# Kernel optimization log

Measured on AMD Instinct MI355X. Metric: run time of the kernel, lower is better.

Reference implementation:

```python
import jax, jax.numpy as jnp
import numpy as np

F_CNT, V_CNT = 1024, 512
H, W = 192, 192
FX, FY = 200.0, 200.0
CX, CY = W / 2.0, H / 2.0
EPS = 1e-8


def quat_to_rot(q):
    # WXYZ quaternion -> rotation matrix, with normalization.
    q = q / (jnp.linalg.norm(q, axis=-1, keepdims=True) + EPS)
    w, x, y, z = q[..., 0], q[..., 1], q[..., 2], q[..., 3]
    return jnp.stack([
        jnp.stack([1 - 2 * (y * y + z * z), 2 * (x * y - w * z), 2 * (x * z + w * y)], -1),
        jnp.stack([2 * (x * y + w * z), 1 - 2 * (x * x + z * z), 2 * (y * z - w * x)], -1),
        jnp.stack([2 * (x * z - w * y), 2 * (y * z + w * x), 1 - 2 * (x * x + y * y)], -1),
    ], -2)


def rot_to_quat(R):
    # Branchless rotation matrix -> WXYZ quaternion.
    m00, m11, m22 = R[..., 0, 0], R[..., 1, 1], R[..., 2, 2]
    qw = 0.5 * jnp.sqrt(jnp.maximum(EPS, 1 + m00 + m11 + m22))
    qx = 0.5 * jnp.sqrt(jnp.maximum(EPS, 1 + m00 - m11 - m22))
    qy = 0.5 * jnp.sqrt(jnp.maximum(EPS, 1 - m00 + m11 - m22))
    qz = 0.5 * jnp.sqrt(jnp.maximum(EPS, 1 - m00 - m11 + m22))
    qx = jnp.copysign(qx, R[..., 2, 1] - R[..., 1, 2])
    qy = jnp.copysign(qy, R[..., 0, 2] - R[..., 2, 0])
    qz = jnp.copysign(qz, R[..., 1, 0] - R[..., 0, 1])
    return jnp.stack([qw, qx, qy, qz], -1)


def get_face_coord(a, b, c):
    # Per-face orthonormal frame (columns = x,y,z axes) and centroid.
    t = (a + b + c) / 3.0
    e1, e2 = b - a, c - a
    x = e1 / (jnp.linalg.norm(e1, axis=-1, keepdims=True) + EPS)
    n = jnp.cross(e1, e2)
    z = n / (jnp.linalg.norm(n, axis=-1, keepdims=True) + EPS)
    y = jnp.cross(z, x)
    return jnp.stack([x, y, z], -1), t


def render_gaussians(means, rot_qs, scales, colors, opac):
    # Differentiable 3DGS-style render: project, build 2D conics, depth-sorted
    # alpha compositing over all gaussians per pixel, white background.
    Rn = quat_to_rot(rot_qs)                      # [F,3,3]
    M = Rn * scales[:, None, :]                   # R @ diag(s)
    cov3 = M @ jnp.swapaxes(M, -1, -2)            # [F,3,3]
    X, Y, Z = means[:, 0], means[:, 1], means[:, 2]
    valid = (Z > 0.2).astype(means.dtype)
    Zc = jnp.maximum(Z, 0.2)
    mx = FX * X / Zc + CX
    my = FY * Y / Zc + CY
    zero = jnp.zeros_like(Zc)
    J = jnp.stack([
        jnp.stack([FX / Zc, zero, -FX * X / (Zc * Zc)], -1),
        jnp.stack([zero, FY / Zc, -FY * Y / (Zc * Zc)], -1),
    ], -2)                                        # [F,2,3]
    cov2 = J @ cov3 @ jnp.swapaxes(J, -1, -2)     # [F,2,2]
    a = cov2[:, 0, 0] + 0.3                       # low-pass dilation (3DGS)
    b = cov2[:, 0, 1]
    c = cov2[:, 1, 1] + 0.3
    det = jnp.maximum(a * c - b * b, EPS)
    conA, conB, conC = c / det, -b / det, a / det
    ys, xs = jnp.meshgrid(jnp.arange(H, dtype=means.dtype),
                          jnp.arange(W, dtype=means.dtype), indexing='ij')
    px, py = xs.reshape(-1), ys.reshape(-1)       # [HW]
    dx = px[None, :] - mx[:, None]                # [F,HW]
    dy = py[None, :] - my[:, None]
    power = -0.5 * (conA[:, None] * dx * dx + conC[:, None] * dy * dy) - conB[:, None] * dx * dy
    alpha = jnp.clip(opac[:, None] * jnp.exp(jnp.minimum(power, 0.0)), 0.0, 0.99) * valid[:, None]
    order = jnp.argsort(Zc)                       # front-to-back
    alpha = alpha[order]
    cols = colors[order]
    T = jnp.cumprod(1.0 - alpha, axis=0)
    T_excl = jnp.concatenate([jnp.ones_like(T[:1]), T[:-1]], axis=0)
    w = alpha * T_excl                            # [F,HW]
    img = jnp.einsum('fp,fc->cp', w, cols) + (1.0 - jnp.sum(w, 0))[None, :]
    return img.reshape(colors.shape[1], H, W)


def setup_inputs() -> dict:
    ks = jax.random.split(jax.random.key(0), 8)
    vp = jax.random.normal(ks[0], (V_CNT, 3), jnp.float32) * 0.5
    vp = vp.at[:, 2].add(5.0)  # put the mesh in front of the camera
    return {
        'img': jax.random.uniform(ks[1], (3, H, W), jnp.float32),
        'mask': jax.random.uniform(ks[2], (H, W), jnp.float32),
        'vertex_positions': vp,
        'faces': jax.random.randint(ks[3], (F_CNT, 3), 0, V_CNT, jnp.int32),
        'gp_rot_qs': jax.random.normal(ks[4], (F_CNT, 4), jnp.float32),
        'gp_log_scales': jax.random.normal(ks[5], (F_CNT, 3), jnp.float32) * 0.1 - 3.0,
        'gp_colors': jax.random.uniform(ks[6], (F_CNT, 3), jnp.float32),
        'gp_log_opacities': jnp.zeros((F_CNT, 1), jnp.float32),
    }


def reference(img, mask, vertex_positions, faces, gp_rot_qs, gp_log_scales,
              gp_colors, gp_log_opacities):
    vps_a = vertex_positions[faces[:, 0]]
    vps_b = vertex_positions[faces[:, 1]]
    vps_c = vertex_positions[faces[:, 2]]
    face_rs, face_ts = get_face_coord(vps_a, vps_b, vps_c)      # [F,3,3],[F,3]
    gp_scales = jnp.exp(gp_log_scales)
    gp_rot_mats = quat_to_rot(gp_rot_qs)
    # rows = scaled columns of the rotation (exactly as the torch code stacks)
    gp_rs = jnp.stack([gp_rot_mats[:, :, 0] * gp_scales[:, 0:1],
                       gp_rot_mats[:, :, 1] * gp_scales[:, 1:2],
                       gp_rot_mats[:, :, 2] * gp_scales[:, 2:3]], -2)
    global_gp_rs = face_rs @ gp_rs                               # merge_rt, gp_t = 0
    global_gp_ts = face_ts
    global_scales = jnp.linalg.norm(global_gp_rs, axis=-2)      # column norms [F,3]
    global_rot = global_gp_rs / (global_scales[:, None, :] + EPS)
    global_qs = rot_to_quat(global_rot)
    opac = jnp.exp(gp_log_opacities)[:, 0]
    rendered = render_gaussians(global_gp_ts, global_qs, global_scales, gp_colors, opac)
    mask_ = mask[None]
    masked_img = (1.0 - mask_) + img * mask_                     # white bg composite
    rgb_loss = jnp.mean((rendered - masked_img) ** 2)
    return rendered, rgb_loss
```

## Files before the change

kernel.cpp:

```cpp
#include <hip/hip_runtime.h>
#include <hip/hip_fp16.h>
#include <math.h>

#define F_CNT 1024
#define H_IMG 192
#define W_IMG 192
#define HW (H_IMG * W_IMG)
#define EPSF 1e-8f
#define N_SEG 8
#define SEG_LEN 128
#define HALF_PX 72
#define PIX_PER_BLK 144
#define LOG2E 1.4426950408889634f

#define RCP(x) __builtin_amdgcn_rcpf(x)


__device__ __forceinline__ void bstep(unsigned long long &kv, int j, int k, int tid)
{
    const unsigned long long pk = __shfl_xor(kv, j, 64);
    const bool keep_min = (((tid & k) == 0) == ((tid & j) == 0));
    kv = ((pk < kv) == keep_min) ? pk : kv;
}

__global__ __launch_bounds__(1024)
void prep_sort_kernel(const float* __restrict__ vp,
                      const int*   __restrict__ faces,
                      const float* __restrict__ rot_qs,
                      const float* __restrict__ log_scales,
                      const float* __restrict__ colors,
                      const float* __restrict__ log_opac,
                      float* __restrict__ params,
                      float* __restrict__ out)
{
    __shared__ float sp[8][F_CNT];
    __shared__ unsigned long long skv[F_CNT];

    const int f = threadIdx.x;
    if (f == 0) out[3 * HW] = 0.0f;

    const int ia = faces[3 * f + 0], ib = faces[3 * f + 1], ic = faces[3 * f + 2];
    const float Ax = vp[3 * ia + 0], Ay = vp[3 * ia + 1], Az = vp[3 * ia + 2];
    const float Bx = vp[3 * ib + 0], By = vp[3 * ib + 1], Bz = vp[3 * ib + 2];
    const float Cx = vp[3 * ic + 0], Cy = vp[3 * ic + 1], Cz = vp[3 * ic + 2];

    const float tx = (Ax + Bx + Cx) / 3.0f;
    const float ty = (Ay + By + Cy) / 3.0f;
    const float tz = (Az + Bz + Cz) / 3.0f;

    const float e1x = Bx - Ax, e1y = By - Ay, e1z = Bz - Az;
    const float e2x = Cx - Ax, e2y = Cy - Ay, e2z = Cz - Az;

    const float rn1 = RCP(sqrtf(e1x * e1x + e1y * e1y + e1z * e1z) + EPSF);
    const float ux = e1x * rn1, uy = e1y * rn1, uz = e1z * rn1;
    const float cnx = e1y * e2z - e1z * e2y;
    const float cny = e1z * e2x - e1x * e2z;
    const float cnz = e1x * e2y - e1y * e2x;
    const float rn2 = RCP(sqrtf(cnx * cnx + cny * cny + cnz * cnz) + EPSF);
    const float wxv = cnx * rn2, wyv = cny * rn2, wzv = cnz * rn2;
    const float vx = wyv * uz - wzv * uy;
    const float vy = wzv * ux - wxv * uz;
    const float vz = wxv * uy - wyv * ux;

    const float q0 = rot_qs[4 * f + 0], q1 = rot_qs[4 * f + 1];
    const float q2 = rot_qs[4 * f + 2], q3 = rot_qs[4 * f + 3];
    const float rqn = RCP(sqrtf(q0 * q0 + q1 * q1 + q2 * q2 + q3 * q3) + EPSF);
    const float qw = q0 * rqn, qx = q1 * rqn, qy = q2 * rqn, qz = q3 * rqn;
    const float R00 = 1.0f - 2.0f * (qy * qy + qz * qz);
    const float R01 = 2.0f * (qx * qy - qw * qz);
    const float R02 = 2.0f * (qx * qz + qw * qy);
    const float R10 = 2.0f * (qx * qy + qw * qz);
    const float R11 = 1.0f - 2.0f * (qx * qx + qz * qz);
    const float R12 = 2.0f * (qy * qz - qw * qx);
    const float R20 = 2.0f * (qx * qz - qw * qy);
    const float R21 = 2.0f * (qy * qz + qw * qx);
    const float R22 = 1.0f - 2.0f * (qx * qx + qy * qy);

    const float s0 = expf(log_scales[3 * f + 0]);
    const float s1 = expf(log_scales[3 * f + 1]);
    const float s2 = expf(log_scales[3 * f + 2]);

    float G00, G10, G20, G01, G11, G21, G02, G12, G22;
    {
        float c0 = s0 * R00, c1 = s1 * R01, c2 = s2 * R02;
        G00 = ux * c0 + vx * c1 + wxv * c2;
        G10 = uy * c0 + vy * c1 + wyv * c2;
        G20 = uz * c0 + vz * c1 + wzv * c2;
    }
    {
        float c0 = s0 * R10, c1 = s1 * R11, c2 = s2 * R12;
        G01 = ux * c0 + vx * c1 + wxv * c2;
        G11 = uy * c0 + vy * c1 + wyv * c2;
        G21 = uz * c0 + vz * c1 + wzv * c2;
    }
    {
        float c0 = s0 * R20, c1 = s1 * R21, c2 = s2 * R22;
        G02 = ux * c0 + vx * c1 + wxv * c2;
        G12 = uy * c0 + vy * c1 + wyv * c2;
        G22 = uz * c0 + vz * c1 + wzv * c2;
    }

    const float gs0 = sqrtf(G00 * G00 + G10 * G10 + G20 * G20);
    const float gs1 = sqrtf(G01 * G01 + G11 * G11 + G21 * G21);
    const float gs2 = sqrtf(G02 * G02 + G12 * G12 + G22 * G22);
    const float rd0 = RCP(gs0 + EPSF), rd1 = RCP(gs1 + EPSF), rd2 = RCP(gs2 + EPSF);
    const float r00 = G00 * rd0, r10 = G10 * rd0, r20 = G20 * rd0;
    const float r01 = G01 * rd1, r11 = G11 * rd1, r21 = G21 * rd1;
    const float r02 = G02 * rd2, r12 = G12 * rd2, r22 = G22 * rd2;

    const float Qw = 0.5f * sqrtf(fmaxf(EPSF, 1.0f + r00 + r11 + r22));
    const float Qx = copysignf(0.5f * sqrtf(fmaxf(EPSF, 1.0f + r00 - r11 - r22)), r21 - r12);
    const float Qy = copysignf(0.5f * sqrtf(fmaxf(EPSF, 1.0f - r00 + r11 - r22)), r02 - r20);
    const float Qz = copysignf(0.5f * sqrtf(fmaxf(EPSF, 1.0f - r00 - r11 + r22)), r10 - r01);

    const float rqn2 = RCP(sqrtf(Qw * Qw + Qx * Qx + Qy * Qy + Qz * Qz) + EPSF);
    const float pw = Qw * rqn2, px = Qx * rqn2, py = Qy * rqn2, pz = Qz * rqn2;
    const float N00 = 1.0f - 2.0f * (py * py + pz * pz);
    const float N01 = 2.0f * (px * py - pw * pz);
    const float N02 = 2.0f * (px * pz + pw * py);
    const float N10 = 2.0f * (px * py + pw * pz);
    const float N11 = 1.0f - 2.0f * (px * px + pz * pz);
    const float N12 = 2.0f * (py * pz - pw * px);
    const float N20 = 2.0f * (px * pz - pw * py);
    const float N21 = 2.0f * (py * pz + pw * px);
    const float N22 = 1.0f - 2.0f * (px * px + py * py);

    const float M00 = N00 * gs0, M01 = N01 * gs1, M02 = N02 * gs2;
    const float M10 = N10 * gs0, M11 = N11 * gs1, M12 = N12 * gs2;
    const float M20 = N20 * gs0, M21 = N21 * gs1, M22 = N22 * gs2;
    const float C00 = M00 * M00 + M01 * M01 + M02 * M02;
    const float C01 = M00 * M10 + M01 * M11 + M02 * M12;
    const float C02 = M00 * M20 + M01 * M21 + M02 * M22;
    const float C11 = M10 * M10 + M11 * M11 + M12 * M12;
    const float C12 = M10 * M20 + M11 * M21 + M12 * M22;
    const float C22 = M20 * M20 + M21 * M21 + M22 * M22;

    const float valid = (tz > 0.2f) ? 1.0f : 0.0f;
    const float Zc = fmaxf(tz, 0.2f);
    const float rZc = RCP(Zc);
    const float mx = 200.0f * tx * rZc + 96.0f;
    const float my = 200.0f * ty * rZc + 96.0f;
    const float j00 = 200.0f * rZc;
    const float j02 = -200.0f * tx * (rZc * rZc);
    const float j11 = 200.0f * rZc;
    const float j12 = -200.0f * ty * (rZc * rZc);
    const float v00 = j00 * j00 * C00 + 2.0f * j00 * j02 * C02 + j02 * j02 * C22 + 0.3f;
    const float v01 = j00 * j11 * C01 + j00 * j12 * C02 + j02 * j11 * C12 + j02 * j12 * C22;
    const float v11 = j11 * j11 * C11 + 2.0f * j11 * j12 * C12 + j12 * j12 * C22 + 0.3f;
    const float rdet = RCP(fmaxf(v00 * v11 - v01 * v01, EPSF));
    const float conA = v11 * rdet, conB = -v01 * rdet, conC = v00 * rdet;
    const float opv = expf(log_opac[f]) * valid;

    const float LA = 0.5f * LOG2E * conA;
    const float LB = LOG2E * conB;
    const float LC = 0.5f * LOG2E * conC;
    const float t4 = fmaf(-LB, LB, 4.0f * LA * LC);
    const float reach2 = 140.0f * LA * RCP(fmaxf(t4, 1e-30f));

    union { __half2 h; float f; } c01u, cbo;
    c01u.h = __floats2half2_rn(colors[3 * f + 0], colors[3 * f + 1]);
    cbo.h  = __floats2half2_rn(colors[3 * f + 2], opv);

    sp[0][f] = mx;
    sp[1][f] = my;
    sp[2][f] = reach2;
    sp[3][f] = LA;
    sp[4][f] = LB;
    sp[5][f] = LC;
    sp[6][f] = c01u.f;
    sp[7][f] = cbo.f;

    unsigned long long kv =
        ((unsigned long long)__float_as_uint(Zc) << 32) | (unsigned int)f;

    #pragma unroll
    for (int k = 2; k <= 64; k <<= 1)
        #pragma unroll
        for (int j = k >> 1; j > 0; j >>= 1)
            bstep(kv, j, k, f);

    skv[f] = kv;
    __syncthreads();

    for (int k = 128; k <= F_CNT; k <<= 1) {
        for (int j = k >> 1; j >= 64; j >>= 1) {
            const int x = f ^ j;
            if (x > f) {
                const unsigned long long a  = skv[f];
                const unsigned long long bb = skv[x];
                const bool up = ((f & k) == 0);
                if (up ? (a > bb) : (a < bb)) { skv[f] = bb; skv[x] = a; }
            }
            __syncthreads();
        }
        kv = skv[f];
        #pragma unroll
        for (int j = 32; j > 0; j >>= 1)
            bstep(kv, j, k, f);
        skv[f] = kv;
        __syncthreads();
    }

    const int src = (int)(skv[f] & 0xffffffffULL);
    float4* __restrict__ d4 = (float4*)params + 2 * f;
    d4[0] = make_float4(sp[0][src], sp[1][src], sp[2][src], sp[3][src]);
    d4[1] = make_float4(sp[4][src], sp[5][src], sp[6][src], sp[7][src]);
}

__global__ __launch_bounds__(512)
void render_kernel(const float* __restrict__ params,
                   const float* __restrict__ img,
                   const float* __restrict__ mask,
                   float* __restrict__ out)
{
    __shared__ float4 lds4[F_CNT * 2];
    __shared__ float  lossb[PIX_PER_BLK];

    const int tid  = threadIdx.x;
    const int lane = tid & 63;
    const int wv   = tid >> 6;

    const float4* __restrict__ rec4 = (const float4*)params;
    #pragma unroll
    for (int k = 0; k < 4; ++k)
        lds4[k * 512 + tid] = rec4[k * 512 + tid];
    __syncthreads();

    const int b   = blockIdx.x;
    const int pb1 = b * HALF_PX;
    const int pb2 = HW / 2 + b * HALF_PX;

    const float r1a = (float)(pb1 / W_IMG);
    const float r1b = (float)((pb1 + HALF_PX - 1) / W_IMG);
    const float r2a = (float)(pb2 / W_IMG);
    const float r2b = (float)((pb2 + HALF_PX - 1) / W_IMG);

    const int p0 = pb1 + lane,      p1 = pb1 + 64 + lane;
    const int p2 = pb2 + lane,      p3 = pb2 + 64 + lane;
    const float fx0 = (float)(p0 % W_IMG), fy0 = (float)(p0 / W_IMG);
    const float fx1 = (float)(p1 % W_IMG), fy1 = (float)(p1 / W_IMG);
    const float fx2 = (float)(p2 % W_IMG), fy2 = (float)(p2 / W_IMG);
    const float fx3 = (float)(p3 % W_IMG), fy3 = (float)(p3 / W_IMG);

    float T0 = 1.0f, R0 = 0.0f, G0 = 0.0f, B0 = 0.0f;
    float T1 = 1.0f, R1 = 0.0f, G1 = 0.0f, B1 = 0.0f;
    float T2 = 1.0f, R2 = 0.0f, G2 = 0.0f, B2 = 0.0f;
    float T3 = 1.0f, R3 = 0.0f, G3 = 0.0f, B3 = 0.0f;

    const float4* __restrict__ Lb = lds4 + (wv << 8);
    for (int i = 0; i < SEG_LEN; ++i) {
        const float4 a = Lb[2 * i + 0];
        const float my = a.y, reach2 = a.z;

        const float dm1 = fmaxf(0.0f, fmaxf(r1a - my, my - r1b));
        const float dm2 = fmaxf(0.0f, fmaxf(r2a - my, my - r2b));
        const bool hit1 = dm1 * dm1 <= reach2;
        const bool hit2 = dm2 * dm2 <= reach2;

        if (hit1 || hit2) {
            const float4 bb = Lb[2 * i + 1];
            const float LA = a.w, LB = bb.x, LC = bb.y;
            union { float f; __half2 h; } urg, ubo;
            urg.f = bb.z;  ubo.f = bb.w;
            const float2 crg = __half22float2(urg.h);
            const float2 cbo = __half22float2(ubo.h);
            const float  cb  = cbo.x, opv = cbo.y;

            if (hit1) {
                {
                    const float dx = fx0 - a.x, dy = fy0 - my;
                    const float t  = fmaf(LB, dy, LA * dx);
                    const float u2 = (LC * dy) * dy;
                    const float n  = -fmaf(t, dx, u2);
                    const float e  = exp2f(fminf(n, 0.0f));
                    const float al = fminf(opv * e, 0.99f);
                    const float w  = al * T0;
                    R0 = fmaf(w, crg.x, R0); G0 = fmaf(w, crg.y, G0); B0 = fmaf(w, cb, B0);
                    T0 -= w;
                }
                {
                    const float dx = fx1 - a.x, dy = fy1 - my;
                    const float t  = fmaf(LB, dy, LA * dx);
                    const float u2 = (LC * dy) * dy;
                    const float n  = -fmaf(t, dx, u2);
                    const float e  = exp2f(fminf(n, 0.0f));
                    const float al = fminf(opv * e, 0.99f);
                    const float w  = al * T1;
                    R1 = fmaf(w, crg.x, R1); G1 = fmaf(w, crg.y, G1); B1 = fmaf(w, cb, B1);
                    T1 -= w;
                }
            }
            if (hit2) {
                {
                    const float dx = fx2 - a.x, dy = fy2 - my;
                    const float t  = fmaf(LB, dy, LA * dx);
                    const float u2 = (LC * dy) * dy;
                    const float n  = -fmaf(t, dx, u2);
                    const float e  = exp2f(fminf(n, 0.0f));
                    const float al = fminf(opv * e, 0.99f);
                    const float w  = al * T2;
                    R2 = fmaf(w, crg.x, R2); G2 = fmaf(w, crg.y, G2); B2 = fmaf(w, cb, B2);
                    T2 -= w;
                }
                {
                    const float dx = fx3 - a.x, dy = fy3 - my;
                    const float t  = fmaf(LB, dy, LA * dx);
                    const float u2 = (LC * dy) * dy;
                    const float n  = -fmaf(t, dx, u2);
                    const float e  = exp2f(fminf(n, 0.0f));
                    const float al = fminf(opv * e, 0.99f);
                    const float w  = al * T3;
                    R3 = fmaf(w, crg.x, R3); G3 = fmaf(w, crg.y, G3); B3 = fmaf(w, cb, B3);
                    T3 -= w;
                }
            }
        }
    }

    __syncthreads();
    float4* __restrict__ fold4 = lds4;
    fold4[wv * PIX_PER_BLK + lane] = make_float4(R0, G0, B0, T0);
    if (lane < 8)
        fold4[wv * PIX_PER_BLK + 64 + lane] = make_float4(R1, G1, B1, T1);
    fold4[wv * PIX_PER_BLK + 72 + lane] = make_float4(R2, G2, B2, T2);
    if (lane < 8)
        fold4[wv * PIX_PER_BLK + 136 + lane] = make_float4(R3, G3, B3, T3);
    __syncthreads();

    float lsum = 0.0f;
    if (tid < PIX_PER_BLK) {
        float R = 0.0f, G = 0.0f, B = 0.0f, Tt = 1.0f;
        #pragma unroll
        for (int s = 0; s < N_SEG; ++s) {
            const float4 c = fold4[s * PIX_PER_BLK + tid];
            R += Tt * c.x; G += Tt * c.y; B += Tt * c.z;
            Tt *= c.w;
        }
        const float bg = Tt;
        const float o0 = R + bg, o1 = G + bg, o2 = B + bg;
        const int p = (tid < HALF_PX) ? (pb1 + tid) : (pb2 + tid - HALF_PX);
        out[p]          = o0;
        out[HW + p]     = o1;
        out[2 * HW + p] = o2;

        const float m = mask[p];
        const float base = 1.0f - m;
        const float e0 = o0 - (base + img[p] * m);
        const float e1 = o1 - (base + img[HW + p] * m);
        const float e2 = o2 - (base + img[2 * HW + p] * m);
        lsum = e0 * e0 + e1 * e1 + e2 * e2;
    }

    if (tid < PIX_PER_BLK) lossb[tid] = lsum;
    __syncthreads();
    if (tid < 64) {
        float s = lossb[tid] + lossb[tid + 64] + (tid < 16 ? lossb[tid + 128] : 0.0f);
        #pragma unroll
        for (int off = 32; off > 0; off >>= 1) s += __shfl_down(s, off);
        if (tid == 0)
            atomicAdd(out + 3 * HW, s * (1.0f / (float)(3 * HW)));
    }
}

extern "C" void kernel_launch(void* const* d_in, const int* in_sizes, int n_in,
                              void* d_out, int out_size, void* d_ws, size_t ws_size,
                              hipStream_t stream)
{
    const float* img        = (const float*)d_in[0];
    const float* mask       = (const float*)d_in[1];
    const float* vp         = (const float*)d_in[2];
    const int*   faces      = (const int*)d_in[3];
    const float* rot_qs     = (const float*)d_in[4];
    const float* log_scales = (const float*)d_in[5];
    const float* colors     = (const float*)d_in[6];
    const float* log_opac   = (const float*)d_in[7];
    float* out    = (float*)d_out;
    float* params = (float*)d_ws;

    prep_sort_kernel<<<1, F_CNT, 0, stream>>>(vp, faces, rot_qs, log_scales,
                                              colors, log_opac, params, out);
    render_kernel<<<(HW / 2) / HALF_PX, 512, 0, stream>>>(params, img, mask, out);
}
```

Baseline: 109.1 us.

## Fuse per-face prep and depth sort into render kernel, recompute per block

Removes the single-block prep/sort kernel and the workspace round-trip. Every render block now recomputes all 1024 face parameters and runs its own bitonic sort with two keys per thread, doing more in registers and shuffles and needing fewer LDS barrier steps. This drops a serial one-block launch and the global params write and read, at the cost of redundant prep and sort work in all 256 blocks and higher LDS use per block. The loss accumulator is now zeroed with a memset instead of inside the prep kernel.

```diff
diff --git a/kernel.cpp b/kernel.cpp
--- a/kernel.cpp
+++ b/kernel.cpp
@@ -16,29 +16,16 @@
 #define RCP(x) __builtin_amdgcn_rcpf(x)
 
 
-__device__ __forceinline__ void bstep(unsigned long long &kv, int j, int k, int tid)
-{
-    const unsigned long long pk = __shfl_xor(kv, j, 64);
-    const bool keep_min = (((tid & k) == 0) == ((tid & j) == 0));
-    kv = ((pk < kv) == keep_min) ? pk : kv;
-}
-
-__global__ __launch_bounds__(1024)
-void prep_sort_kernel(const float* __restrict__ vp,
-                      const int*   __restrict__ faces,
-                      const float* __restrict__ rot_qs,
-                      const float* __restrict__ log_scales,
-                      const float* __restrict__ colors,
-                      const float* __restrict__ log_opac,
-                      float* __restrict__ params,
-                      float* __restrict__ out)
-{
-    __shared__ float sp[8][F_CNT];
-    __shared__ unsigned long long skv[F_CNT];
-
-    const int f = threadIdx.x;
-    if (f == 0) out[3 * HW] = 0.0f;
-
+__device__ __forceinline__ unsigned long long prep_face(
+    const int f,
+    const float* __restrict__ vp,
+    const int*   __restrict__ faces,
+    const float* __restrict__ rot_qs,
+    const float* __restrict__ log_scales,
+    const float* __restrict__ colors,
+    const float* __restrict__ log_opac,
+    float sp[8][F_CNT])
+{
     const int ia = faces[3 * f + 0], ib = faces[3 * f + 1], ic = faces[3 * f + 2];
     const float Ax = vp[3 * ia + 0], Ay = vp[3 * ia + 1], Az = vp[3 * ia + 2];
     const float Bx = vp[3 * ib + 0], By = vp[3 * ib + 1], Bz = vp[3 * ib + 2];
@@ -170,49 +157,41 @@
     sp[6][f] = c01u.f;
     sp[7][f] = cbo.f;
 
-    unsigned long long kv =
-        ((unsigned long long)__float_as_uint(Zc) << 32) | (unsigned int)f;
-
-    #pragma unroll
-    for (int k = 2; k <= 64; k <<= 1)
-        #pragma unroll
-        for (int j = k >> 1; j > 0; j >>= 1)
-            bstep(kv, j, k, f);
-
-    skv[f] = kv;
-    __syncthreads();
-
-    for (int k = 128; k <= F_CNT; k <<= 1) {
-        for (int j = k >> 1; j >= 64; j >>= 1) {
-            const int x = f ^ j;
-            if (x > f) {
-                const unsigned long long a  = skv[f];
-                const unsigned long long bb = skv[x];
-                const bool up = ((f & k) == 0);
-                if (up ? (a > bb) : (a < bb)) { skv[f] = bb; skv[x] = a; }
-            }
-            __syncthreads();
-        }
-        kv = skv[f];
-        #pragma unroll
-        for (int j = 32; j > 0; j >>= 1)
-            bstep(kv, j, k, f);
-        skv[f] = kv;
-        __syncthreads();
-    }
-
-    const int src = (int)(skv[f] & 0xffffffffULL);
-    float4* __restrict__ d4 = (float4*)params + 2 * f;
-    d4[0] = make_float4(sp[0][src], sp[1][src], sp[2][src], sp[3][src]);
-    d4[1] = make_float4(sp[4][src], sp[5][src], sp[6][src], sp[7][src]);
+    return ((unsigned long long)__float_as_uint(Zc) << 32) | (unsigned int)f;
+}
+
+__device__ __forceinline__ unsigned long long bpick(unsigned long long own,
+                                                    unsigned long long part,
+                                                    bool keep_min)
+{
+    return ((part < own) == keep_min) ? part : own;
+}
+
+__device__ __forceinline__ void rstep2(unsigned long long &k0,
+                                       unsigned long long &k1,
+                                       int d , int kh ,
+                                       int t)
+{
+    const unsigned long long p0 = __shfl_xor(k0, d, 64);
+    const unsigned long long p1 = __shfl_xor(k1, d, 64);
+    const bool keep_min = (((t & kh) == 0) == ((t & d) == 0));
+    k0 = bpick(k0, p0, keep_min);
+    k1 = bpick(k1, p1, keep_min);
 }
 
 __global__ __launch_bounds__(512)
-void render_kernel(const float* __restrict__ params,
-                   const float* __restrict__ img,
-                   const float* __restrict__ mask,
-                   float* __restrict__ out)
-{
+void fused_kernel(const float* __restrict__ vp,
+                  const int*   __restrict__ faces,
+                  const float* __restrict__ rot_qs,
+                  const float* __restrict__ log_scales,
+                  const float* __restrict__ colors,
+                  const float* __restrict__ log_opac,
+                  const float* __restrict__ img,
+                  const float* __restrict__ mask,
+                  float* __restrict__ out)
+{
+    __shared__ float  sp[8][F_CNT];
+    __shared__ unsigned long long skv[F_CNT];
     __shared__ float4 lds4[F_CNT * 2];
     __shared__ float  lossb[PIX_PER_BLK];
 
@@ -220,10 +199,46 @@
     const int lane = tid & 63;
     const int wv   = tid >> 6;
 
-    const float4* __restrict__ rec4 = (const float4*)params;
+    unsigned long long k0 = prep_face(2 * tid,     vp, faces, rot_qs,
+                                      log_scales, colors, log_opac, sp);
+    unsigned long long k1 = prep_face(2 * tid + 1, vp, faces, rot_qs,
+                                      log_scales, colors, log_opac, sp);
+
     #pragma unroll
-    for (int k = 0; k < 4; ++k)
-        lds4[k * 512 + tid] = rec4[k * 512 + tid];
+    for (int k = 2; k <= 128; k <<= 1) {
+        #pragma unroll
+        for (int j = k >> 1; j >= 2; j >>= 1)
+            rstep2(k0, k1, j >> 1, k >> 1, tid);
+        const bool up = ((tid & (k >> 1)) == 0);
+        if ((k0 > k1) == up) { unsigned long long tt = k0; k0 = k1; k1 = tt; }
+    }
+    for (int k = 256; k <= F_CNT; k <<= 1) {
+        for (int j = k >> 1; j >= 128; j >>= 1) {
+            skv[2 * tid]     = k0;
+            skv[2 * tid + 1] = k1;
+            __syncthreads();
+            const unsigned long long p0 = skv[(2 * tid)     ^ j];
+            const unsigned long long p1 = skv[(2 * tid + 1) ^ j];
+            __syncthreads();
+            const bool keep_min = ((((2 * tid) & k) == 0) == (((2 * tid) & j) == 0));
+            k0 = bpick(k0, p0, keep_min);
+            k1 = bpick(k1, p1, keep_min);
+        }
+        #pragma unroll
+        for (int j = 64; j >= 2; j >>= 1)
+            rstep2(k0, k1, j >> 1, k >> 1, tid);
+        const bool up = ((tid & (k >> 1)) == 0);
+        if ((k0 > k1) == up) { unsigned long long tt = k0; k0 = k1; k1 = tt; }
+    }
+
+    {
+        const int s0 = (int)(k0 & 0xffffffffULL);
+        const int s1 = (int)(k1 & 0xffffffffULL);
+        lds4[4 * tid + 0] = make_float4(sp[0][s0], sp[1][s0], sp[2][s0], sp[3][s0]);
+        lds4[4 * tid + 1] = make_float4(sp[4][s0], sp[5][s0], sp[6][s0], sp[7][s0]);
+        lds4[4 * tid + 2] = make_float4(sp[0][s1], sp[1][s1], sp[2][s1], sp[3][s1]);
+        lds4[4 * tid + 3] = make_float4(sp[4][s1], sp[5][s1], sp[6][s1], sp[7][s1]);
+    }
     __syncthreads();
 
     const int b   = blockIdx.x;
@@ -374,10 +389,10 @@
     const float* log_scales = (const float*)d_in[5];
     const float* colors     = (const float*)d_in[6];
     const float* log_opac   = (const float*)d_in[7];
-    float* out    = (float*)d_out;
-    float* params = (float*)d_ws;
-
-    prep_sort_kernel<<<1, F_CNT, 0, stream>>>(vp, faces, rot_qs, log_scales,
-                                              colors, log_opac, params, out);
-    render_kernel<<<(HW / 2) / HALF_PX, 512, 0, stream>>>(params, img, mask, out);
-}
+    float* out = (float*)d_out;
+
+    hipMemsetAsync(out + 3 * HW, 0, sizeof(float), stream);
+
+    fused_kernel<<<(HW / 2) / HALF_PX, 512, 0, stream>>>(
+        vp, faces, rot_qs, log_scales, colors, log_opac, img, mask, out);
+}
```

Measured after the change: 108.8 us. No clear change (-0.3%).

## Fuse prep/sort into render kernel and compact per-wave hit lists

Applied to the files above, without the earlier changes.

Merges the single-block preprocessing and sort kernel into the render kernel. Every render block now redundantly recomputes face parameters and runs the full bitonic sort in LDS, which removes the second launch and the global round-trip of the params buffer. Each block also uses 1024 threads, one wave per segment-and-strip pair, and builds a compacted list of the gaussians whose reach touches its rows via ballot and popcount. The loop then runs only over those hits instead of testing all 128. The cost is doing the sort 256 times, more LDS per block, and a host memset to zero the loss accumulator.

```diff
diff --git a/kernel.cpp b/kernel.cpp
--- a/kernel.cpp
+++ b/kernel.cpp
@@ -16,29 +16,16 @@
 #define RCP(x) __builtin_amdgcn_rcpf(x)
 
 
-__device__ __forceinline__ void bstep(unsigned long long &kv, int j, int k, int tid)
+__device__ __forceinline__ unsigned long long prep_face(
+    const int f,
+    const float* __restrict__ vp,
+    const int*   __restrict__ faces,
+    const float* __restrict__ rot_qs,
+    const float* __restrict__ log_scales,
+    const float* __restrict__ colors,
+    const float* __restrict__ log_opac,
+    float sp[8][F_CNT])
 {
-    const unsigned long long pk = __shfl_xor(kv, j, 64);
-    const bool keep_min = (((tid & k) == 0) == ((tid & j) == 0));
-    kv = ((pk < kv) == keep_min) ? pk : kv;
-}
-
-__global__ __launch_bounds__(1024)
-void prep_sort_kernel(const float* __restrict__ vp,
-                      const int*   __restrict__ faces,
-                      const float* __restrict__ rot_qs,
-                      const float* __restrict__ log_scales,
-                      const float* __restrict__ colors,
-                      const float* __restrict__ log_opac,
-                      float* __restrict__ params,
-                      float* __restrict__ out)
-{
-    __shared__ float sp[8][F_CNT];
-    __shared__ unsigned long long skv[F_CNT];
-
-    const int f = threadIdx.x;
-    if (f == 0) out[3 * HW] = 0.0f;
-
     const int ia = faces[3 * f + 0], ib = faces[3 * f + 1], ic = faces[3 * f + 2];
     const float Ax = vp[3 * ia + 0], Ay = vp[3 * ia + 1], Az = vp[3 * ia + 2];
     const float Bx = vp[3 * ib + 0], By = vp[3 * ib + 1], Bz = vp[3 * ib + 2];
@@ -170,161 +157,161 @@
     sp[6][f] = c01u.f;
     sp[7][f] = cbo.f;
 
-    unsigned long long kv =
-        ((unsigned long long)__float_as_uint(Zc) << 32) | (unsigned int)f;
+    return ((unsigned long long)__float_as_uint(Zc) << 32) | (unsigned int)f;
+}
+
+__device__ __forceinline__ void bstep(unsigned long long &kv, int j, int k, int tid)
+{
+    const unsigned long long pk = __shfl_xor(kv, j, 64);
+    const bool keep_min = (((tid & k) == 0) == ((tid & j) == 0));
+    kv = ((pk < kv) == keep_min) ? pk : kv;
+}
+
+__global__ __launch_bounds__(1024)
+void fused_kernel(const float* __restrict__ vp,
+                  const int*   __restrict__ faces,
+                  const float* __restrict__ rot_qs,
+                  const float* __restrict__ log_scales,
+                  const float* __restrict__ colors,
+                  const float* __restrict__ log_opac,
+                  const float* __restrict__ img,
+                  const float* __restrict__ mask,
+                  float* __restrict__ out)
+{
+    __shared__ float  sp[8][F_CNT];
+    __shared__ unsigned long long skv[F_CNT];
+    __shared__ float4 lds4[F_CNT * 2];
+    __shared__ unsigned int hlist[16][SEG_LEN];
+    __shared__ float  lossb[PIX_PER_BLK];
+
+    const int tid  = threadIdx.x;
+    const int lane = tid & 63;
+    const int wv   = tid >> 6;
+
+    unsigned long long kv = prep_face(tid, vp, faces, rot_qs,
+                                      log_scales, colors, log_opac, sp);
 
     #pragma unroll
     for (int k = 2; k <= 64; k <<= 1)
         #pragma unroll
         for (int j = k >> 1; j > 0; j >>= 1)
-            bstep(kv, j, k, f);
-
-    skv[f] = kv;
+            bstep(kv, j, k, tid);
+
+    skv[tid] = kv;
     __syncthreads();
 
     for (int k = 128; k <= F_CNT; k <<= 1) {
         for (int j = k >> 1; j >= 64; j >>= 1) {
-            const int x = f ^ j;
-            if (x > f) {
-                const unsigned long long a  = skv[f];
+            const int x = tid ^ j;
+            if (x > tid) {
+                const unsigned long long a  = skv[tid];
                 const unsigned long long bb = skv[x];
-                const bool up = ((f & k) == 0);
-                if (up ? (a > bb) : (a < bb)) { skv[f] = bb; skv[x] = a; }
+                const bool up = ((tid & k) == 0);
+                if (up ? (a > bb) : (a < bb)) { skv[tid] = bb; skv[x] = a; }
             }
             __syncthreads();
         }
-        kv = skv[f];
+        kv = skv[tid];
         #pragma unroll
         for (int j = 32; j > 0; j >>= 1)
-            bstep(kv, j, k, f);
-        skv[f] = kv;
+            bstep(kv, j, k, tid);
+        skv[tid] = kv;
         __syncthreads();
     }
 
-    const int src = (int)(skv[f] & 0xffffffffULL);
-    float4* __restrict__ d4 = (float4*)params + 2 * f;
-    d4[0] = make_float4(sp[0][src], sp[1][src], sp[2][src], sp[3][src]);
-    d4[1] = make_float4(sp[4][src], sp[5][src], sp[6][src], sp[7][src]);
-}
-
-__global__ __launch_bounds__(512)
-void render_kernel(const float* __restrict__ params,
-                   const float* __restrict__ img,
-                   const float* __restrict__ mask,
-                   float* __restrict__ out)
-{
-    __shared__ float4 lds4[F_CNT * 2];
-    __shared__ float  lossb[PIX_PER_BLK];
-
-    const int tid  = threadIdx.x;
-    const int lane = tid & 63;
-    const int wv   = tid >> 6;
-
-    const float4* __restrict__ rec4 = (const float4*)params;
-    #pragma unroll
-    for (int k = 0; k < 4; ++k)
-        lds4[k * 512 + tid] = rec4[k * 512 + tid];
+    {
+        const int src = (int)(skv[tid] & 0xffffffffULL);
+        lds4[2 * tid + 0] = make_float4(sp[0][src], sp[1][src], sp[2][src], sp[3][src]);
+        lds4[2 * tid + 1] = make_float4(sp[4][src], sp[5][src], sp[6][src], sp[7][src]);
+        ((float2*)skv)[tid] = make_float2(sp[1][src], sp[2][src]);
+    }
     __syncthreads();
 
     const int b   = blockIdx.x;
     const int pb1 = b * HALF_PX;
     const int pb2 = HW / 2 + b * HALF_PX;
-
-    const float r1a = (float)(pb1 / W_IMG);
-    const float r1b = (float)((pb1 + HALF_PX - 1) / W_IMG);
-    const float r2a = (float)(pb2 / W_IMG);
-    const float r2b = (float)((pb2 + HALF_PX - 1) / W_IMG);
-
-    const int p0 = pb1 + lane,      p1 = pb1 + 64 + lane;
-    const int p2 = pb2 + lane,      p3 = pb2 + 64 + lane;
+    const int seg = wv & 7;
+    const bool strip2 = (wv >= 8);
+    const int pbase = strip2 ? pb2 : pb1;
+
+    const float ra = (float)(pbase / W_IMG);
+    const float rb = (float)((pbase + HALF_PX - 1) / W_IMG);
+
+    int nhit;
+    {
+        const float4 tt = ((const float4*)skv)[seg * 64 + lane];
+
+        const float dmA = fmaxf(0.0f, fmaxf(ra - tt.x, tt.x - rb));
+        const float dmB = fmaxf(0.0f, fmaxf(ra - tt.z, tt.z - rb));
+        const bool hA = dmA * dmA <= tt.y;
+        const bool hB = dmB * dmB <= tt.w;
+
+        const unsigned long long m0 = __ballot(hA);
+        const unsigned long long m1 = __ballot(hB);
+        const unsigned long long lt = (1ULL << lane) - 1ULL;
+        const int pos0 = __popcll(m0 & lt) + __popcll(m1 & lt);
+        const int pos1 = pos0 + (hA ? 1 : 0);
+        if (hA) hlist[wv][pos0] = (unsigned)(2 * lane);
+        if (hB) hlist[wv][pos1] = (unsigned)(2 * lane + 1);
+        nhit = __popcll(m0) + __popcll(m1);
+    }
+    __syncthreads();
+
+    const int p0 = pbase + lane, p1 = pbase + 64 + lane;
     const float fx0 = (float)(p0 % W_IMG), fy0 = (float)(p0 / W_IMG);
     const float fx1 = (float)(p1 % W_IMG), fy1 = (float)(p1 / W_IMG);
-    const float fx2 = (float)(p2 % W_IMG), fy2 = (float)(p2 / W_IMG);
-    const float fx3 = (float)(p3 % W_IMG), fy3 = (float)(p3 / W_IMG);
 
     float T0 = 1.0f, R0 = 0.0f, G0 = 0.0f, B0 = 0.0f;
     float T1 = 1.0f, R1 = 0.0f, G1 = 0.0f, B1 = 0.0f;
-    float T2 = 1.0f, R2 = 0.0f, G2 = 0.0f, B2 = 0.0f;
-    float T3 = 1.0f, R3 = 0.0f, G3 = 0.0f, B3 = 0.0f;
-
-    const float4* __restrict__ Lb = lds4 + (wv << 8);
-    for (int i = 0; i < SEG_LEN; ++i) {
-        const float4 a = Lb[2 * i + 0];
-        const float my = a.y, reach2 = a.z;
-
-        const float dm1 = fmaxf(0.0f, fmaxf(r1a - my, my - r1b));
-        const float dm2 = fmaxf(0.0f, fmaxf(r2a - my, my - r2b));
-        const bool hit1 = dm1 * dm1 <= reach2;
-        const bool hit2 = dm2 * dm2 <= reach2;
-
-        if (hit1 || hit2) {
-            const float4 bb = Lb[2 * i + 1];
-            const float LA = a.w, LB = bb.x, LC = bb.y;
-            union { float f; __half2 h; } urg, ubo;
-            urg.f = bb.z;  ubo.f = bb.w;
-            const float2 crg = __half22float2(urg.h);
-            const float2 cbo = __half22float2(ubo.h);
-            const float  cb  = cbo.x, opv = cbo.y;
-
-            if (hit1) {
-                {
-                    const float dx = fx0 - a.x, dy = fy0 - my;
-                    const float t  = fmaf(LB, dy, LA * dx);
-                    const float u2 = (LC * dy) * dy;
-                    const float n  = -fmaf(t, dx, u2);
-                    const float e  = exp2f(fminf(n, 0.0f));
-                    const float al = fminf(opv * e, 0.99f);
-                    const float w  = al * T0;
-                    R0 = fmaf(w, crg.x, R0); G0 = fmaf(w, crg.y, G0); B0 = fmaf(w, cb, B0);
-                    T0 -= w;
-                }
-                {
-                    const float dx = fx1 - a.x, dy = fy1 - my;
-                    const float t  = fmaf(LB, dy, LA * dx);
-                    const float u2 = (LC * dy) * dy;
-                    const float n  = -fmaf(t, dx, u2);
-                    const float e  = exp2f(fminf(n, 0.0f));
-                    const float al = fminf(opv * e, 0.99f);
-                    const float w  = al * T1;
-                    R1 = fmaf(w, crg.x, R1); G1 = fmaf(w, crg.y, G1); B1 = fmaf(w, cb, B1);
-                    T1 -= w;
-                }
-            }
-            if (hit2) {
-                {
-                    const float dx = fx2 - a.x, dy = fy2 - my;
-                    const float t  = fmaf(LB, dy, LA * dx);
-                    const float u2 = (LC * dy) * dy;
-                    const float n  = -fmaf(t, dx, u2);
-                    const float e  = exp2f(fminf(n, 0.0f));
-                    const float al = fminf(opv * e, 0.99f);
-                    const float w  = al * T2;
-                    R2 = fmaf(w, crg.x, R2); G2 = fmaf(w, crg.y, G2); B2 = fmaf(w, cb, B2);
-                    T2 -= w;
-                }
-                {
-                    const float dx = fx3 - a.x, dy = fy3 - my;
-                    const float t  = fmaf(LB, dy, LA * dx);
-                    const float u2 = (LC * dy) * dy;
-                    const float n  = -fmaf(t, dx, u2);
-                    const float e  = exp2f(fminf(n, 0.0f));
-                    const float al = fminf(opv * e, 0.99f);
-                    const float w  = al * T3;
-                    R3 = fmaf(w, crg.x, R3); G3 = fmaf(w, crg.y, G3); B3 = fmaf(w, cb, B3);
-                    T3 -= w;
-                }
-            }
+
+    const float4* __restrict__ Lb = lds4 + (seg << 8);
+    for (int i = 0; i < nhit; ++i) {
+        const int r = (int)hlist[wv][i];
+        const float4 a  = Lb[2 * r + 0];
+        const float4 bb = Lb[2 * r + 1];
+        const float my = a.y;
+        const float LA = a.w, LB = bb.x, LC = bb.y;
+        union { float f; __half2 h; } urg, ubo;
+        urg.f = bb.z;  ubo.f = bb.w;
+        const float2 crg = __half22float2(urg.h);
+        const float2 cbo = __half22float2(ubo.h);
+        const float  cb  = cbo.x, opv = cbo.y;
+
+        {
+            const float dx = fx0 - a.x, dy = fy0 - my;
+            const float t  = fmaf(LB, dy, LA * dx);
+            const float u2 = (LC * dy) * dy;
+            const float n  = -fmaf(t, dx, u2);
+            const float e2 = exp2f(fminf(n, 0.0f));
+            const float al = fminf(opv * e2, 0.99f);
+            const float w  = al * T0;
+            R0 = fmaf(w, crg.x, R0); G0 = fmaf(w, crg.y, G0); B0 = fmaf(w, cb, B0);
+            T0 -= w;
         }
+        {
+            const float dx = fx1 - a.x, dy = fy1 - my;
+            const float t  = fmaf(LB, dy, LA * dx);
+            const float u2 = (LC * dy) * dy;
+            const float n  = -fmaf(t, dx, u2);
+            const float e2 = exp2f(fminf(n, 0.0f));
+            const float al = fminf(opv * e2, 0.99f);
+            const float w  = al * T1;
+            R1 = fmaf(w, crg.x, R1); G1 = fmaf(w, crg.y, G1); B1 = fmaf(w, cb, B1);
+            T1 -= w;
+        }
     }
 
     __syncthreads();
     float4* __restrict__ fold4 = lds4;
-    fold4[wv * PIX_PER_BLK + lane] = make_float4(R0, G0, B0, T0);
-    if (lane < 8)
-        fold4[wv * PIX_PER_BLK + 64 + lane] = make_float4(R1, G1, B1, T1);
-    fold4[wv * PIX_PER_BLK + 72 + lane] = make_float4(R2, G2, B2, T2);
-    if (lane < 8)
-        fold4[wv * PIX_PER_BLK + 136 + lane] = make_float4(R3, G3, B3, T3);
+    if (!strip2) {
+        fold4[seg * PIX_PER_BLK + lane] = make_float4(R0, G0, B0, T0);
+        if (lane < 8)
+            fold4[seg * PIX_PER_BLK + 64 + lane] = make_float4(R1, G1, B1, T1);
+    } else {
+        fold4[seg * PIX_PER_BLK + 72 + lane] = make_float4(R0, G0, B0, T0);
+        if (lane < 8)
+            fold4[seg * PIX_PER_BLK + 136 + lane] = make_float4(R1, G1, B1, T1);
+    }
     __syncthreads();
 
     float lsum = 0.0f;
@@ -374,10 +361,10 @@
     const float* log_scales = (const float*)d_in[5];
     const float* colors     = (const float*)d_in[6];
     const float* log_opac   = (const float*)d_in[7];
-    float* out    = (float*)d_out;
-    float* params = (float*)d_ws;
-
-    prep_sort_kernel<<<1, F_CNT, 0, stream>>>(vp, faces, rot_qs, log_scales,
-                                              colors, log_opac, params, out);
-    render_kernel<<<(HW / 2) / HALF_PX, 512, 0, stream>>>(params, img, mask, out);
+    float* out = (float*)d_out;
+
+    hipMemsetAsync(out + 3 * HW, 0, sizeof(float), stream);
+
+    fused_kernel<<<(HW / 2) / HALF_PX, 1024, 0, stream>>>(
+        vp, faces, rot_qs, log_scales, colors, log_opac, img, mask, out);
 }
```

Result: faster. 101.0 us (-7.4%).
